# Kernel tuning notes

Hardware: AMD Instinct MI355X
Metric: run time of the kernel (lower is better)

Reference implementation:

```python
import jax, jax.numpy as jnp
import numpy as np

B, N1, N2, C, P, H, MLP = 8, 4096, 4096, 512, 256, 8, 2048
HD = C // H  # head dim = 64
EPS = 1e-12


def _l2norm(x):
    # torch F.normalize(dim=-1): x / max(||x||_2, eps)
    n = jnp.sqrt(jnp.sum(x * x, axis=-1, keepdims=True))
    return x / jnp.maximum(n, EPS)


def setup_inputs() -> dict:
    key = jax.random.key(0)
    ks = jax.random.split(key, 8)
    w = lambda i, shape: jax.random.normal(ks[i], shape, jnp.float32) * 0.02
    return {
        "x1": jax.random.normal(ks[0], (B, N1, C), jnp.float32),
        "x2": jax.random.normal(ks[1], (B, N2, C), jnp.float32),
        "Wq": w(2, (C, C)), "bq": jnp.zeros((C,), jnp.float32),
        "Wkv": w(3, (C, 2 * C)), "bkv": jnp.zeros((2 * C,), jnp.float32),
        # proj_k and proj_v share ONE Linear(N_2, proj_size) in the source
        "Wp": w(4, (N2, P)), "bp": jnp.zeros((P,), jnp.float32),
        "pos_q": jnp.zeros((1, N1, C), jnp.float32),
        "pos_k": jnp.zeros((1, N2, C), jnp.float32),
        "temperature": jnp.ones((H, 1, 1), jnp.float32),
        "W1": w(5, (C, MLP)), "b1": jnp.zeros((MLP,), jnp.float32),
        "W2": w(6, (MLP, C)), "b2": jnp.zeros((C,), jnp.float32),
    }


def reference(x1, x2, Wq, bq, Wkv, bkv, Wp, bp, pos_q, pos_k, temperature,
              W1, b1, W2, b2):
    # q += pos_embed_q is in-place in torch, so q_skip includes pos embedding
    q = x1 @ Wq + bq + pos_q                      # [B,N1,C]
    q_skip = q
    kv = x2 @ Wkv + bkv                           # [B,N2,2C]
    k = kv[..., :C] + pos_k                       # [B,N2,C]
    v = kv[..., C:]                               # [B,N2,C]

    qh = q.reshape(B, N1, H, HD).transpose(0, 2, 1, 3)   # [B,H,N1,hd]
    kh = k.reshape(B, N2, H, HD).transpose(0, 2, 1, 3)   # [B,H,N2,hd]
    vh = v.reshape(B, N2, H, HD).transpose(0, 2, 1, 3)   # [B,H,N2,hd]

    # project K^T and V^T along the sequence axis (shared weights)
    kp = jnp.einsum('bhnd,np->bhdp', kh, Wp) + bp        # [B,H,hd,P]
    vp_t = jnp.einsum('bhnd,np->bhdp', vh, Wp) + bp      # [B,H,hd,P]

    attn = jnp.einsum('bhqd,bhdp->bhqp', qh, kp) * temperature  # [B,H,N1,P]
    attn = jax.nn.softmax(attn, axis=-1)                 # dropout: eval mode

    x = jnp.einsum('bhqp,bhdp->bhqd', attn, vp_t)        # [B,H,N1,hd]
    # source does permute(0,3,1,2).reshape(B,N1,C) -- replicate exactly
    x = x.transpose(0, 3, 1, 2).reshape(B, N1, C)

    x = _l2norm(x + q_skip)                              # Add & L2-Norm
    h = jax.nn.gelu(x @ W1 + b1, approximate=False)      # nn.GELU (exact)
    out = _l2norm(h @ W2 + b2 + x)                       # FFN -> Add & L2-Norm
    return out
```

## Files before the change

kernel.cpp:

```cpp
#include <hip/hip_runtime.h>
#include <hip/hip_bf16.h>
#include <math.h>

#define B_    8
#define N1_   4096
#define N2_   4096
#define C_    512
#define P_    256
#define H_    8
#define MLP_  2048
#define HD_   64

typedef __hip_bfloat16 bf16;
typedef __attribute__((ext_vector_type(8))) short short8;
typedef __attribute__((ext_vector_type(4))) float f32x4;

__device__ __forceinline__ float bf2f(bf16 v) { return __bfloat162float(v); }
__device__ __forceinline__ bf16  f2bf(float v) { return __float2bfloat16(v); }
__device__ __forceinline__ float ubf2f(unsigned short u) {
  union { float f; unsigned int i; } cv; cv.i = ((unsigned int)u) << 16; return cv.f;
}
__device__ __forceinline__ unsigned short f2bfu(float v) {
  union { bf16 b; unsigned short u; } cv; cv.b = __float2bfloat16(v); return cv.u;
}
__device__ __forceinline__ float gelu_exact(float x) {
  return 0.5f * x * (1.0f + erff(x * 0.70710678118654752f));
}

__device__ __forceinline__ void gload16(const void* g, void* l) {
  __builtin_amdgcn_global_load_lds(
      (const __attribute__((address_space(1))) void*)g,
      (__attribute__((address_space(3))) void*)l, 16, 0, 0);
}

__global__ __launch_bounds__(256) void f2b_kernel(
    const float* __restrict__ in, bf16* __restrict__ out, int n4)
{
  int i = blockIdx.x * 256 + threadIdx.x;
  const int stride = gridDim.x * 256;
  for (; i < n4; i += stride) {
    const float4 v = ((const float4*)in)[i];
    ushort4 o;
    o.x = f2bfu(v.x); o.y = f2bfu(v.y); o.z = f2bfu(v.z); o.w = f2bfu(v.w);
    ((ushort4*)out)[i] = o;
  }
}

__global__ __launch_bounds__(256) void transpose_f2b_kernel(
    const float* __restrict__ in, bf16* __restrict__ out, int K, int N, int ldin)
{
  __shared__ float tile[32][33];
  const int kb = blockIdx.y * 32, nb = blockIdx.x * 32;
  const int tx = threadIdx.x & 31, ty = threadIdx.x >> 5;
  #pragma unroll
  for (int i = 0; i < 4; ++i)
    tile[ty + 8 * i][tx] = in[(size_t)(kb + ty + 8 * i) * ldin + nb + tx];
  __syncthreads();
  #pragma unroll
  for (int i = 0; i < 4; ++i)
    out[(size_t)(nb + ty + 8 * i) * K + kb + tx] = f2bf(tile[tx][ty + 8 * i]);
}

__global__ __launch_bounds__(256) void transpose_bf16_kernel(
    const bf16* __restrict__ in, bf16* __restrict__ out, int R, int Cc)
{
  __shared__ unsigned short tile[64][80];
  const size_t ib = (size_t)blockIdx.z * R * Cc;
  const int rb = blockIdx.y * 64, cb = blockIdx.x * 64;
  const int tr = threadIdx.x >> 3, ch = threadIdx.x & 7;
  #pragma unroll
  for (int p = 0; p < 2; ++p) {
    const int r = tr + 32 * p;
    const short8 v = *(const short8*)(in + ib + (size_t)(rb + r) * Cc + cb + ch * 8);
    *(short8*)&tile[r][ch * 8] = v;
  }
  __syncthreads();
  #pragma unroll
  for (int p = 0; p < 2; ++p) {
    const int c = tr + 32 * p;
    short8 v;
    #pragma unroll
    for (int e = 0; e < 8; ++e) v[e] = (short)tile[ch * 8 + e][c];
    *(short8*)(out + ib + (size_t)(cb + c) * R + rb + ch * 8) = v;
  }
}

template<int BN, int OUTF32, int ACT, int POS>
__global__ __launch_bounds__(256) void mfma_gemm_kernel(
    const bf16* __restrict__ A, const bf16* __restrict__ Bt,
    const float* __restrict__ bias, const float* __restrict__ pos, int posmask,
    void* __restrict__ Cv, int M, int N, int K)
{
  constexpr int WGN = BN / 64;
  constexpr int WGR = 4 / WGN;
  constexpr int FM  = 128 / (16 * WGR);
  __shared__ bf16 As[128 * 32];
  __shared__ bf16 Bs[BN * 32];
  const int t  = threadIdx.x;
  const int l  = t & 63;
  const int w  = t >> 6;
  const int wr = w / WGN, wc = w % WGN;
  const int lr = l & 15, kg = l >> 4;
  const int m0 = blockIdx.y * 128, n0 = blockIdx.x * BN;

  const bf16* ga = A  + (size_t)(m0 + (t >> 2)) * K + (t & 3) * 8;
  const bf16* gb = Bt + (size_t)(n0 + (t >> 2)) * K + (t & 3) * 8;
  char* asl = (char*)As + t * 16;
  char* bsl = (char*)Bs + t * 16;

  f32x4 acc[FM][4] = {};

  for (int k0 = 0; k0 < K; k0 += 32) {
    gload16(ga, asl);
    gload16(ga + (size_t)64 * K, asl + 4096);
    gload16(gb, bsl);
    if (BN == 128) gload16(gb + (size_t)64 * K, bsl + 4096);
    ga += 32; gb += 32;
    __syncthreads();
    short8 af[FM], bfv[4];
    #pragma unroll
    for (int i = 0; i < FM; ++i)
      af[i] = *(const short8*)&As[(wr * (FM * 16) + i * 16 + lr) * 32 + kg * 8];
    #pragma unroll
    for (int j = 0; j < 4; ++j)
      bfv[j] = *(const short8*)&Bs[(wc * 64 + j * 16 + lr) * 32 + kg * 8];
    #pragma unroll
    for (int i = 0; i < FM; ++i)
      #pragma unroll
      for (int j = 0; j < 4; ++j)
        acc[i][j] = __builtin_amdgcn_mfma_f32_16x16x32_bf16(
            af[i], bfv[j], acc[i][j], 0, 0, 0);
    __syncthreads();
  }

  #pragma unroll
  for (int i = 0; i < FM; ++i) {
    #pragma unroll
    for (int j = 0; j < 4; ++j) {
      const int n = n0 + wc * 64 + j * 16 + lr;
      const float bv = bias[n];
      #pragma unroll
      for (int r = 0; r < 4; ++r) {
        const int m = m0 + wr * (FM * 16) + i * 16 + kg * 4 + r;
        float v = acc[i][j][r] + bv;
        if (POS) v += pos[(size_t)(m & posmask) * N + n];
        if (ACT) v = gelu_exact(v);
        if (OUTF32) ((float*)Cv)[(size_t)m * N + n] = v;
        else        ((bf16*)Cv)[(size_t)m * N + n] = f2bf(v);
      }
    }
  }
}

template<int BIASM>
__global__ __launch_bounds__(256) void proj_kernel(
    const bf16* __restrict__ A, const bf16* __restrict__ Bt,
    const float* __restrict__ bias, bf16* __restrict__ Cb,
    int M, int N, int K, long aBatch, long bBatch, long cBatch)
{
  __shared__ bf16 As[64 * 32];
  __shared__ bf16 Bs[64 * 32];
  const int t = threadIdx.x, l = t & 63, w = t >> 6;
  const int wr = w >> 1, wc = w & 1;
  const int lr = l & 15, kg = l >> 4;
  const int z = blockIdx.z;
  const int m0 = blockIdx.y * 64, n0 = blockIdx.x * 64;
  const bf16* ga = A  + (size_t)z * aBatch + (size_t)(m0 + (t >> 2)) * K + (t & 3) * 8;
  const bf16* gb = Bt + (size_t)z * bBatch + (size_t)(n0 + (t >> 2)) * K + (t & 3) * 8;
  char* asl = (char*)As + t * 16;
  char* bsl = (char*)Bs + t * 16;
  f32x4 acc[2][2] = {};
  for (int k0 = 0; k0 < K; k0 += 32) {
    gload16(ga, asl);
    gload16(gb, bsl);
    ga += 32; gb += 32;
    __syncthreads();
    short8 af[2], bfr[2];
    #pragma unroll
    for (int i = 0; i < 2; ++i)
      af[i] = *(const short8*)&As[(wr * 32 + i * 16 + lr) * 32 + kg * 8];
    #pragma unroll
    for (int j = 0; j < 2; ++j)
      bfr[j] = *(const short8*)&Bs[(wc * 32 + j * 16 + lr) * 32 + kg * 8];
    #pragma unroll
    for (int i = 0; i < 2; ++i)
      #pragma unroll
      for (int j = 0; j < 2; ++j)
        acc[i][j] = __builtin_amdgcn_mfma_f32_16x16x32_bf16(
            af[i], bfr[j], acc[i][j], 0, 0, 0);
    __syncthreads();
  }
  #pragma unroll
  for (int i = 0; i < 2; ++i)
    #pragma unroll
    for (int j = 0; j < 2; ++j) {
      const int n = n0 + wc * 32 + j * 16 + lr;
      #pragma unroll
      for (int r = 0; r < 4; ++r) {
        const int m = m0 + wr * 32 + i * 16 + kg * 4 + r;
        const float v = acc[i][j][r] + (BIASM ? bias[m] : bias[n]);
        Cb[(size_t)z * cBatch + (size_t)m * N + n] = f2bf(v);
      }
    }
}

__global__ __launch_bounds__(256) void attn_mfma_kernel(
    const bf16* __restrict__ qb, const bf16* __restrict__ kpT,
    const bf16* __restrict__ vp, const float* __restrict__ temp,
    bf16* __restrict__ xat)
{
  __shared__ bf16 qs[64 * 64];
  __shared__ bf16 us[256 * 64];
  __shared__ bf16 vs[64 * 256];
  const int t = threadIdx.x, w = t >> 6, l = t & 63;
  const int lr = l & 15, kg = l >> 4;
  const int b = blockIdx.z, h = blockIdx.y;
  const int q0 = blockIdx.x * 64;
  const int bh = b * H_ + h;
  const float tv = temp[h];

  {
    const int rowb = t >> 3, ch = t & 7;
    #pragma unroll
    for (int p = 0; p < 2; ++p) {
      const int r = rowb + 32 * p;
      const short8 v = *(const short8*)(qb + ((size_t)(b * N1_ + q0 + r)) * C_ + h * HD_ + ch * 8);
      *(short8*)((char*)qs + ((r * 128 + ch * 16) ^ ((r & 7) << 4))) = v;
    }
    const bf16* kpb = kpT + (size_t)bh * (P_ * HD_);
    #pragma unroll
    for (int p = 0; p < 8; ++p) {
      const int r = rowb + 32 * p;
      const short8 v = *(const short8*)(kpb + r * HD_ + ch * 8);
      *(short8*)((char*)us + ((r * 128 + ch * 16) ^ ((r & 7) << 4))) = v;
    }
    const bf16* vpb = vp + (size_t)bh * (HD_ * P_);
    const int rowv = t >> 5, chv = t & 31;
    #pragma unroll
    for (int p = 0; p < 8; ++p) {
      const int r = rowv + 8 * p;
      const short8 v = *(const short8*)(vpb + r * P_ + chv * 8);
      *(short8*)((char*)vs + ((r * 512 + chv * 16) ^ ((r & 7) << 4))) = v;
    }
  }
  __syncthreads();

  short8 aq[2];
  {
    const int row = w * 16 + lr;
    const int sw = (row & 7) << 4;
    aq[0] = *(const short8*)((const char*)qs + ((row * 128 +  0 + kg * 16) ^ sw));
    aq[1] = *(const short8*)((const char*)qs + ((row * 128 + 64 + kg * 16) ^ sw));
  }
  f32x4 s[16] = {};
  #pragma unroll
  for (int j = 0; j < 16; ++j) {
    const int row = j * 16 + lr;
    const int sw = (row & 7) << 4;
    const short8 b0 = *(const short8*)((const char*)us + ((row * 128 +  0 + kg * 16) ^ sw));
    const short8 b1 = *(const short8*)((const char*)us + ((row * 128 + 64 + kg * 16) ^ sw));
    s[j] = __builtin_amdgcn_mfma_f32_16x16x32_bf16(aq[0], b0, s[j], 0, 0, 0);
    s[j] = __builtin_amdgcn_mfma_f32_16x16x32_bf16(aq[1], b1, s[j], 0, 0, 0);
  }

  float inv_[4];
  #pragma unroll
  for (int j = 0; j < 16; ++j)
    #pragma unroll
    for (int r = 0; r < 4; ++r) s[j][r] *= tv;
  #pragma unroll
  for (int r = 0; r < 4; ++r) {
    float m = s[0][r];
    #pragma unroll
    for (int j = 1; j < 16; ++j) m = fmaxf(m, s[j][r]);
    #pragma unroll
    for (int off = 1; off < 16; off <<= 1) m = fmaxf(m, __shfl_xor(m, off));
    float sum = 0.f;
    #pragma unroll
    for (int j = 0; j < 16; ++j) { s[j][r] = __expf(s[j][r] - m); sum += s[j][r]; }
    #pragma unroll
    for (int off = 1; off < 16; off <<= 1) sum += __shfl_xor(sum, off);
    inv_[r] = 1.0f / sum;
  }
  __syncthreads();

  #pragma unroll
  for (int r = 0; r < 4; ++r) {
    const int q = w * 16 + kg * 4 + r;
    const int sw = (q & 7) << 4;
    #pragma unroll
    for (int j = 0; j < 16; ++j) {
      const int p = j * 16 + lr;
      ((unsigned short*)us)[((q * 512 + p * 2) ^ sw) >> 1] = f2bfu(s[j][r] * inv_[r]);
    }
  }
  __syncthreads();

  f32x4 o[4] = {};
  #pragma unroll
  for (int kc = 0; kc < 8; ++kc) {
    const int qrow = w * 16 + lr;
    const short8 pb = *(const short8*)((const char*)us +
        ((qrow * 512 + kc * 64 + kg * 16) ^ ((qrow & 7) << 4)));
    #pragma unroll
    for (int i = 0; i < 4; ++i) {
      const int drow = i * 16 + lr;
      const short8 vb = *(const short8*)((const char*)vs +
          ((drow * 512 + kc * 64 + kg * 16) ^ ((drow & 7) << 4)));
      o[i] = __builtin_amdgcn_mfma_f32_16x16x32_bf16(vb, pb, o[i], 0, 0, 0);
    }
  }
  const size_t obase = ((size_t)bh * N1_ + q0 + w * 16 + lr) * HD_;
  #pragma unroll
  for (int i = 0; i < 4; ++i) {
    ushort4 pk;
    pk.x = f2bfu(o[i][0]); pk.y = f2bfu(o[i][1]);
    pk.z = f2bfu(o[i][2]); pk.w = f2bfu(o[i][3]);
    *(ushort4*)((bf16*)xat + obase + i * 16 + kg * 4) = pk;
  }
}

__global__ __launch_bounds__(256) void norm1_kernel(
    const bf16* __restrict__ xat, const bf16* __restrict__ qb,
    bf16* __restrict__ xb)
{
  const int row = blockIdx.x;
  const int b = row >> 12, np = row & 4095;
  const int d = np >> 6, h = (np >> 3) & 7, qhi = np & 7;
  const int c0 = threadIdx.x, c1 = threadIdx.x + 256;
  const size_t sbase = (size_t)((b * H_ + h) * N1_ + qhi * 512);
  float v0 = bf2f(xat[(sbase + c0) * HD_ + d]) + bf2f(qb[(size_t)row * C_ + c0]);
  float v1 = bf2f(xat[(sbase + c1) * HD_ + d]) + bf2f(qb[(size_t)row * C_ + c1]);
  float ss = v0 * v0 + v1 * v1;
  #pragma unroll
  for (int off = 32; off > 0; off >>= 1) ss += __shfl_xor(ss, off);
  __shared__ float sw[4];
  if ((threadIdx.x & 63) == 0) sw[threadIdx.x >> 6] = ss;
  __syncthreads();
  const float tot = sw[0] + sw[1] + sw[2] + sw[3];
  const float scale = 1.0f / fmaxf(sqrtf(tot), 1e-12f);
  xb[(size_t)row * C_ + c0] = f2bf(v0 * scale);
  xb[(size_t)row * C_ + c1] = f2bf(v1 * scale);
}

__global__ __launch_bounds__(256) void norm2_kernel(
    const float* __restrict__ yb, const bf16* __restrict__ xb,
    float* __restrict__ outp)
{
  const int row = blockIdx.x;
  const int c0 = threadIdx.x, c1 = threadIdx.x + 256;
  float v0 = yb[(size_t)row * C_ + c0] + bf2f(xb[(size_t)row * C_ + c0]);
  float v1 = yb[(size_t)row * C_ + c1] + bf2f(xb[(size_t)row * C_ + c1]);
  float ss = v0 * v0 + v1 * v1;
  #pragma unroll
  for (int off = 32; off > 0; off >>= 1) ss += __shfl_xor(ss, off);
  __shared__ float sw[4];
  if ((threadIdx.x & 63) == 0) sw[threadIdx.x >> 6] = ss;
  __syncthreads();
  const float tot = sw[0] + sw[1] + sw[2] + sw[3];
  const float scale = 1.0f / fmaxf(sqrtf(tot), 1e-12f);
  outp[(size_t)row * C_ + c0] = v0 * scale;
  outp[(size_t)row * C_ + c1] = v1 * scale;
}

extern "C" void kernel_launch(void* const* d_in, const int* in_sizes, int n_in,
                              void* d_out, int out_size, void* d_ws, size_t ws_size,
                              hipStream_t stream)
{
  const float* x1   = (const float*)d_in[0];
  const float* x2   = (const float*)d_in[1];
  const float* Wq   = (const float*)d_in[2];
  const float* bq   = (const float*)d_in[3];
  const float* Wkv  = (const float*)d_in[4];
  const float* bkv  = (const float*)d_in[5];
  const float* Wp   = (const float*)d_in[6];
  const float* bp   = (const float*)d_in[7];
  const float* posq = (const float*)d_in[8];
  const float* posk = (const float*)d_in[9];
  const float* temp = (const float*)d_in[10];
  const float* W1   = (const float*)d_in[11];
  const float* b1   = (const float*)d_in[12];
  const float* W2   = (const float*)d_in[13];
  const float* b2   = (const float*)d_in[14];

  char* ws = (char*)d_ws;
  bf16*  Abuf = (bf16*)(ws);
  bf16*  Bbuf = (bf16*)(ws + 33554432);
  bf16*  Cbuf = (bf16*)(ws + 67108864);
  bf16*  kpT  = (bf16*)(ws + 100663296);
  bf16*  vpb  = (bf16*)(ws + 102760448);
  bf16*  WpT  = (bf16*)(ws + 104857600);
  bf16*  W1t  = (bf16*)(ws + 100663296);
  bf16*  W2t  = (bf16*)(ws + 102760448);
  bf16*  Wqt  = (bf16*)(ws + 106954752);
  bf16*  Wkt  = (bf16*)(ws + 107479040);
  bf16*  Wvt  = (bf16*)(ws + 108003328);
  float* yb   = (float*)(ws + 106954752);
  float* outp = (float*)d_out;

  const dim3 blk(256);
  const int Mrows = B_ * N1_;
  const int CH = 8192;
  bf16* xat = Bbuf;
  bf16* xb  = Abuf;
  bf16* hb  = Bbuf;
  bf16* qb  = Cbuf;

  f2b_kernel<<<dim3(2048), blk, 0, stream>>>(x2, Abuf, (B_ * N2_ * C_) / 4);
  transpose_f2b_kernel<<<dim3(16, 16), blk, 0, stream>>>(Wkv,      Wkt, C_, C_, 2 * C_);
  transpose_f2b_kernel<<<dim3(16, 16), blk, 0, stream>>>(Wkv + C_, Wvt, C_, C_, 2 * C_);
  transpose_f2b_kernel<<<dim3(16, 16), blk, 0, stream>>>(Wq,       Wqt, C_, C_, C_);
  transpose_f2b_kernel<<<dim3(8, 128), blk, 0, stream>>>(Wp,       WpT, N2_, P_, P_);

  mfma_gemm_kernel<128,0,0,1><<<dim3(C_/128, Mrows/128), blk, 0, stream>>>(
      Abuf, Wkt, bkv, posk, N2_ - 1, Bbuf, Mrows, C_, C_);
  transpose_bf16_kernel<<<dim3(C_/64, N2_/64, B_), blk, 0, stream>>>(
      Bbuf, Cbuf, N2_, C_);
  proj_kernel<1><<<dim3(1, 4, B_*H_), blk, 0, stream>>>(
      WpT, Cbuf, bp, kpT, P_, HD_, N2_, 0L, (long)HD_*N2_, (long)P_*HD_);
  mfma_gemm_kernel<128,0,0,0><<<dim3(C_/128, Mrows/128), blk, 0, stream>>>(
      Abuf, Wvt, bkv + C_, nullptr, 0, Bbuf, Mrows, C_, C_);
  transpose_bf16_kernel<<<dim3(C_/64, N2_/64, B_), blk, 0, stream>>>(
      Bbuf, Cbuf, N2_, C_);
  proj_kernel<0><<<dim3(4, 1, B_*H_), blk, 0, stream>>>(
      Cbuf, WpT, bp, vpb, HD_, P_, N2_, (long)HD_*N2_, 0L, (long)HD_*P_);
  f2b_kernel<<<dim3(2048), blk, 0, stream>>>(x1, Abuf, (B_ * N1_ * C_) / 4);
  mfma_gemm_kernel<128,0,0,1><<<dim3(C_/128, Mrows/128), blk, 0, stream>>>(
      Abuf, Wqt, bq, posq, N1_ - 1, qb, Mrows, C_, C_);
  attn_mfma_kernel<<<dim3(N1_/64, H_, B_), blk, 0, stream>>>(
      qb, kpT, vpb, temp, xat);
  transpose_f2b_kernel<<<dim3(64, 16), blk, 0, stream>>>(W1, W1t, C_,   MLP_, MLP_);
  transpose_f2b_kernel<<<dim3(16, 64), blk, 0, stream>>>(W2, W2t, MLP_, C_,   C_);
  norm1_kernel<<<dim3(Mrows), blk, 0, stream>>>(xat, qb, xb);
  for (int c = 0; c < Mrows / CH; ++c) {
    const bf16* xc = xb + (size_t)c * CH * C_;
    mfma_gemm_kernel<128,0,1,0><<<dim3(MLP_/128, CH/128), blk, 0, stream>>>(
        xc, W1t, b1, nullptr, 0, hb, CH, MLP_, C_);
    mfma_gemm_kernel<64,1,0,0><<<dim3(C_/64, CH/128), blk, 0, stream>>>(
        hb, W2t, b2, nullptr, 0, yb, CH, C_, MLP_);
    norm2_kernel<<<dim3(CH), blk, 0, stream>>>(
        yb, xc, outp + (size_t)c * CH * C_);
  }
}
```

Measured before the change: 933.8 us.

## Store attention output d-major for coalesced norm1 reads; enlarge FFN chunks

The attention kernel now writes its output transposed ([bh, d, q] instead of [bh, q, d]). norm1 can then read two contiguous bf16 values per thread instead of doing strided gathers with a 64-element stride. The attention store becomes a strided scalar scatter across d rows, though the 16 lanes sharing a d still write contiguous q positions. Separately, when the workspace is large enough, the FFN loop runs over larger row chunks with fewer launches, with the weight and yb buffers relocated to fit.

New measurement: 835.6 us. 1.12x faster.

```diff
diff --git a/kernel.cpp b/kernel.cpp
--- a/kernel.cpp
+++ b/kernel.cpp
@@ -207,7 +207,7 @@
 __global__ __launch_bounds__(256) void attn_mfma_kernel(
     const bf16* __restrict__ qb, const bf16* __restrict__ kpT,
     const bf16* __restrict__ vp, const float* __restrict__ temp,
-    bf16* __restrict__ xat)
+    bf16* __restrict__ xatT)
 {
   __shared__ bf16 qs[64 * 64];
   __shared__ bf16 us[256 * 64];
@@ -310,27 +310,31 @@
       o[i] = __builtin_amdgcn_mfma_f32_16x16x32_bf16(vb, pb, o[i], 0, 0, 0);
     }
   }
-  const size_t obase = ((size_t)bh * N1_ + q0 + w * 16 + lr) * HD_;
-  #pragma unroll
-  for (int i = 0; i < 4; ++i) {
-    ushort4 pk;
-    pk.x = f2bfu(o[i][0]); pk.y = f2bfu(o[i][1]);
-    pk.z = f2bfu(o[i][2]); pk.w = f2bfu(o[i][3]);
-    *(ushort4*)((bf16*)xat + obase + i * 16 + kg * 4) = pk;
-  }
+  const int qq = q0 + w * 16 + lr;
+  bf16* ob = xatT + (size_t)bh * (HD_ * (size_t)N1_) + qq;
+  #pragma unroll
+  for (int i = 0; i < 4; ++i)
+    #pragma unroll
+    for (int r = 0; r < 4; ++r) {
+      const int d = i * 16 + kg * 4 + r;
+      ob[(size_t)d * N1_] = f2bf(o[i][r]);
+    }
 }
 
 __global__ __launch_bounds__(256) void norm1_kernel(
-    const bf16* __restrict__ xat, const bf16* __restrict__ qb,
+    const bf16* __restrict__ xatT, const bf16* __restrict__ qb,
     bf16* __restrict__ xb)
 {
   const int row = blockIdx.x;
   const int b = row >> 12, np = row & 4095;
   const int d = np >> 6, h = (np >> 3) & 7, qhi = np & 7;
-  const int c0 = threadIdx.x, c1 = threadIdx.x + 256;
-  const size_t sbase = (size_t)((b * H_ + h) * N1_ + qhi * 512);
-  float v0 = bf2f(xat[(sbase + c0) * HD_ + d]) + bf2f(qb[(size_t)row * C_ + c0]);
-  float v1 = bf2f(xat[(sbase + c1) * HD_ + d]) + bf2f(qb[(size_t)row * C_ + c1]);
+  const int c = threadIdx.x * 2;
+  const size_t tbase = ((size_t)(b * H_ + h) * HD_ + d) * N1_ + qhi * 512 + c;
+  const size_t qbase = (size_t)row * C_ + c;
+  const ushort2 xa = *(const ushort2*)((const unsigned short*)xatT + tbase);
+  const ushort2 qa = *(const ushort2*)((const unsigned short*)qb + qbase);
+  float v0 = ubf2f(xa.x) + ubf2f(qa.x);
+  float v1 = ubf2f(xa.y) + ubf2f(qa.y);
   float ss = v0 * v0 + v1 * v1;
   #pragma unroll
   for (int off = 32; off > 0; off >>= 1) ss += __shfl_xor(ss, off);
@@ -339,8 +343,10 @@
   __syncthreads();
   const float tot = sw[0] + sw[1] + sw[2] + sw[3];
   const float scale = 1.0f / fmaxf(sqrtf(tot), 1e-12f);
-  xb[(size_t)row * C_ + c0] = f2bf(v0 * scale);
-  xb[(size_t)row * C_ + c1] = f2bf(v1 * scale);
+  ushort2 o;
+  o.x = f2bfu(v0 * scale);
+  o.y = f2bfu(v1 * scale);
+  *(ushort2*)((unsigned short*)xb + qbase) = o;
 }
 
 __global__ __launch_bounds__(256) void norm2_kernel(
@@ -390,21 +396,30 @@
   bf16*  kpT  = (bf16*)(ws + 100663296);
   bf16*  vpb  = (bf16*)(ws + 102760448);
   bf16*  WpT  = (bf16*)(ws + 104857600);
-  bf16*  W1t  = (bf16*)(ws + 100663296);
-  bf16*  W2t  = (bf16*)(ws + 102760448);
   bf16*  Wqt  = (bf16*)(ws + 106954752);
   bf16*  Wkt  = (bf16*)(ws + 107479040);
   bf16*  Wvt  = (bf16*)(ws + 108003328);
-  float* yb   = (float*)(ws + 106954752);
   float* outp = (float*)d_out;
+
+  int CH;
+  size_t w1t_off, w2t_off, yb_off;
+  if (ws_size >= 239075328UL) {
+    CH = 32768; w1t_off = 167772160UL; w2t_off = 169869312UL; yb_off = 171966464UL;
+  } else if (ws_size >= 138412032UL) {
+    CH = 16384; w1t_off = 100663296UL; w2t_off = 102760448UL; yb_off = 104857600UL;
+  } else {
+    CH = 8192;  w1t_off = 100663296UL; w2t_off = 102760448UL; yb_off = 106954752UL;
+  }
+  bf16*  W1t = (bf16*)(ws + w1t_off);
+  bf16*  W2t = (bf16*)(ws + w2t_off);
+  float* yb  = (float*)(ws + yb_off);
 
   const dim3 blk(256);
   const int Mrows = B_ * N1_;
-  const int CH = 8192;
-  bf16* xat = Bbuf;
-  bf16* xb  = Abuf;
-  bf16* hb  = Bbuf;
-  bf16* qb  = Cbuf;
+  bf16* xatT = Bbuf;
+  bf16* xb   = Abuf;
+  bf16* hb   = Bbuf;
+  bf16* qb   = Cbuf;
 
   f2b_kernel<<<dim3(2048), blk, 0, stream>>>(x2, Abuf, (B_ * N2_ * C_) / 4);
   transpose_f2b_kernel<<<dim3(16, 16), blk, 0, stream>>>(Wkv,      Wkt, C_, C_, 2 * C_);
@@ -428,10 +443,10 @@
   mfma_gemm_kernel<128,0,0,1><<<dim3(C_/128, Mrows/128), blk, 0, stream>>>(
       Abuf, Wqt, bq, posq, N1_ - 1, qb, Mrows, C_, C_);
   attn_mfma_kernel<<<dim3(N1_/64, H_, B_), blk, 0, stream>>>(
-      qb, kpT, vpb, temp, xat);
+      qb, kpT, vpb, temp, xatT);
   transpose_f2b_kernel<<<dim3(64, 16), blk, 0, stream>>>(W1, W1t, C_,   MLP_, MLP_);
   transpose_f2b_kernel<<<dim3(16, 64), blk, 0, stream>>>(W2, W2t, MLP_, C_,   C_);
-  norm1_kernel<<<dim3(Mrows), blk, 0, stream>>>(xat, qb, xb);
+  norm1_kernel<<<dim3(Mrows), blk, 0, stream>>>(xatT, qb, xb);
   for (int c = 0; c < Mrows / CH; ++c) {
     const bf16* xc = xb + (size_t)c * CH * C_;
     mfma_gemm_kernel<128,0,1,0><<<dim3(MLP_/128, CH/128), blk, 0, stream>>>(
```
